# Optimization experiments

Hardware: AMD Instinct MI355X
Metric: run time of the kernel (lower is better)

The kernel has to match this reference:

```python
import jax, jax.numpy as jnp
import numpy as np

NUM_REP = 3

def setup_inputs() -> dict:
    N, E, DIM, R2, L, B, NEG = 20000, 100000, 32, 100, 4, 4, 32
    ks = jax.random.split(jax.random.key(0), 12)
    # all negatives in a row share the same head (required by the model's assert)
    h = jax.random.randint(ks[0], (B, 1), 0, N)
    t = jax.random.randint(ks[1], (B, NEG), 0, N)
    batch = jnp.stack([jnp.broadcast_to(h, (B, NEG)), t], axis=-1)  # [B,NEG,2]
    edge_index = jax.random.randint(ks[2], (2, E), 0, N)
    edge_type = jax.random.randint(ks[3], (E,), 0, R2)
    edge_attr = 0.1 * jax.random.normal(ks[4], (E, DIM), jnp.float32)
    start_query = jax.random.normal(ks[5], (NUM_REP, DIM), jnp.float32)
    W_rel = jax.random.normal(ks[6], (L, DIM, R2 * DIM), jnp.float32) * (DIM ** -0.5)
    b_rel = jnp.zeros((L, R2 * DIM), jnp.float32)
    W_lin = jax.random.normal(ks[7], (L, 2 * DIM, DIM), jnp.float32) * ((2 * DIM) ** -0.5)
    b_lin = jnp.zeros((L, DIM), jnp.float32)
    W_mlp1 = jax.random.normal(ks[8], (DIM, DIM), jnp.float32) * (DIM ** -0.5)
    b_mlp1 = jnp.zeros((DIM,), jnp.float32)
    W_mlp2 = jax.random.normal(ks[9], (DIM, DIM), jnp.float32) * (DIM ** -0.5)
    b_mlp2 = jnp.zeros((DIM,), jnp.float32)
    return {"batch": batch, "edge_index": edge_index, "edge_type": edge_type,
            "edge_attr": edge_attr, "num_nodes": N, "start_query": start_query,
            "W_rel": W_rel, "b_rel": b_rel, "W_lin": W_lin, "b_lin": b_lin,
            "W_mlp1": W_mlp1, "b_mlp1": b_mlp1, "W_mlp2": W_mlp2, "b_mlp2": b_mlp2}

def reference(batch, edge_index, edge_type, edge_attr, num_nodes, start_query,
              W_rel, b_rel, W_lin, b_lin, W_mlp1, b_mlp1, W_mlp2, b_mlp2):
    B, num_neg, _ = batch.shape
    N = int(num_nodes)
    dim = start_query.shape[1]
    L = W_rel.shape[0]
    bs = NUM_REP * B
    batch_full = jnp.tile(batch, (NUM_REP, 1, 1))            # [bs, neg, 2]
    query_idx = jnp.repeat(jnp.arange(NUM_REP), B)           # [bs]
    h_index, t_index = batch_full[..., 0], batch_full[..., 1]
    # negative_sample_to_tail (no-op when heads are constant per row, as built)
    is_t_neg = jnp.all(h_index == h_index[:, :1], axis=-1, keepdims=True)
    h_index, t_index = (jnp.where(is_t_neg, h_index, t_index),
                        jnp.where(is_t_neg, t_index, h_index))
    h0 = h_index[:, 0]
    q = start_query[query_idx]                               # [bs, dim]
    rows = jnp.arange(bs)
    boundary = jnp.zeros((bs, N, dim), q.dtype).at[rows, h0].add(q)
    pb = jnp.zeros((bs, N), q.dtype).at[rows, h0].set(1.0)   # path boundary
    src, dst = edge_index[0], edge_index[1]
    x = boundary
    for l in range(L):
        # dependent per-query relation embeddings: [bs, 2R, dim]
        rel = (q @ W_rel[l] + b_rel[l]).reshape(bs, -1, dim)
        rel_e = rel[:, edge_type] + edge_attr[None]          # [bs, E, dim]
        msg = x[:, src] * rel_e                              # distmult message
        # sum aggregation; boundary acts as the self-loop message
        agg = jnp.zeros((bs, N, dim), x.dtype).at[:, dst].add(msg) + boundary
        x = jax.nn.relu(jnp.concatenate([x, agg], axis=-1) @ W_lin[l] + b_lin[l])
        # reachability propagation of the path boundary (scatter-max)
        pb = jnp.maximum(pb, jnp.zeros((bs, N), pb.dtype).at[:, dst].max(pb[:, src]))
    feat_t = x[rows[:, None], t_index]                       # [bs, neg, dim]
    feat = feat_t.reshape(NUM_REP, B, num_neg, dim).mean(0)  # mean over reps
    features = jax.nn.relu(feat @ W_mlp1 + b_mlp1) @ W_mlp2 + b_mlp2
    pb_t = pb[rows[:, None], t_index][..., None]             # [bs, neg, 1]
    path_boundary = pb_t.reshape(NUM_REP, B, num_neg, 1).max(0)
    return features, path_boundary
```

## Files before the change

### kernel.cpp

```cpp
#include <hip/hip_runtime.h>

#define N_NODES 20000
#define N_EDGES 100000
#define DIM 32
#define R2 100
#define NLAYERS 4
#define BATCH 4
#define NEG 32
#define NREP 3
#define BS (NREP * BATCH)
#define RELDIM (R2 * DIM)

#define NPB 4
#define TPN 96
#define LBLK (NPB * TPN)
#define GRID_LAYER (N_NODES / NPB)

#define XO_A 0
#define XO_B (XO_A + (size_t)N_NODES * BS * DIM)
#define PBO_A (XO_B + (size_t)N_NODES * BS * DIM)
#define PBO_B (PBO_A + (size_t)N_NODES * BS)
#define RELO (PBO_B + (size_t)N_NODES * BS)
#define QO (RELO + (size_t)NLAYERS * R2 * BS * DIM)
#define FLOAT_TOTAL (QO + (size_t)BS * DIM)

#define IO_H0 0
#define IO_TIDX (IO_H0 + BS)
#define IO_COUNTS (IO_TIDX + BS * NEG)
#define IO_OFF (IO_COUNTS + N_NODES)
#define IO_BCUR (IO_OFF + N_NODES + 1)
#define IO_CURSOR (IO_BCUR + 256)
#define IO_ORDER (IO_CURSOR + N_NODES)
#define IO_PAD (IO_ORDER + N_NODES)
#define IO_ES (((IO_PAD + 1) / 2) * 2)
#define INT_TOTAL (IO_ES + 2 * N_EDGES)

__global__ void k_init(const int* __restrict__ batch,
                       const float* __restrict__ start_query,
                       float* __restrict__ q, int* __restrict__ h0,
                       int* __restrict__ t_idx) {
    int r = threadIdx.x;
    if (r >= BS) return;
    int b = r % BATCH, rep = r / BATCH;
    int h00 = batch[(b * NEG + 0) * 2 + 0];
    bool is_t_neg = true;
    for (int j = 0; j < NEG; j++)
        if (batch[(b * NEG + j) * 2 + 0] != h00) { is_t_neg = false; break; }
    int hsel = is_t_neg ? 0 : 1;
    int h0v = batch[(b * NEG + 0) * 2 + hsel];
    h0[r] = h0v;
    for (int j = 0; j < NEG; j++)
        t_idx[r * NEG + j] = batch[(b * NEG + j) * 2 + (1 - hsel)];
    for (int d = 0; d < DIM; d++) q[r * DIM + d] = start_query[rep * DIM + d];
}

__global__ void k_count(const int* __restrict__ dst, int* __restrict__ counts) {
    int e = blockIdx.x * blockDim.x + threadIdx.x;
    if (e < N_EDGES) atomicAdd(&counts[dst[e]], 1);
}

__global__ void k_scan(const int* __restrict__ counts, int* __restrict__ off,
                       int* __restrict__ cursor, int* __restrict__ bcursor) {
    __shared__ int sd[1024];
    __shared__ int hist[256];
    int t = threadIdx.x;
    const int CH = (N_NODES + 1023) / 1024;
    int base = t * CH;
    for (int i = t; i < 256; i += 1024) hist[i] = 0;
    int sum = 0;
    for (int i = 0; i < CH; i++) {
        int idx = base + i;
        if (idx < N_NODES) sum += counts[idx];
    }
    sd[t] = sum;
    __syncthreads();
    for (int o = 1; o < 1024; o <<= 1) {
        int v = (t >= o) ? sd[t - o] : 0;
        __syncthreads();
        sd[t] += v;
        __syncthreads();
    }
    int excl = sd[t] - sum;
    int run = excl;
    for (int i = 0; i < CH; i++) {
        int idx = base + i;
        if (idx < N_NODES) {
            int c = counts[idx];
            off[idx] = run;
            cursor[idx] = run;
            run += c;
            atomicAdd(&hist[c < 255 ? c : 255], 1);
        }
    }
    if (t == 1023) off[N_NODES] = sd[1023];
    __syncthreads();
    if (t == 0) {
        int acc = 0;
        for (int b = 0; b < 256; b++) { bcursor[b] = acc; acc += hist[b]; }
    }
}

__global__ void k_place(const int* __restrict__ src, const int* __restrict__ dst,
                        const int* __restrict__ etype, int* __restrict__ cursor,
                        int2* __restrict__ es) {
    int e = blockIdx.x * blockDim.x + threadIdx.x;
    if (e < N_EDGES) {
        int p = atomicAdd(&cursor[dst[e]], 1);
        es[p] = make_int2(src[e] | (etype[e] << 20), e);
    }
}

__global__ void k_order(const int* __restrict__ counts, int* __restrict__ bcursor,
                        int* __restrict__ node_order) {
    int n = blockIdx.x * blockDim.x + threadIdx.x;
    if (n < N_NODES) {
        int deg = counts[n]; if (deg > 255) deg = 255;
        int pos = atomicAdd(&bcursor[deg], 1);
        node_order[pos] = n;
    }
}

__global__ void k_rel_all(const float* __restrict__ q, const float* __restrict__ W_rel,
                          const float* __restrict__ b_rel, float* __restrict__ rel) {
    int idx = blockIdx.x * blockDim.x + threadIdx.x;
    if (idx >= NLAYERS * R2 * BS * DIM) return;
    int d = idx & 31;
    int r = (idx >> 5) % BS;
    int et = (idx / (BS * DIM)) % R2;
    int l = idx / (R2 * BS * DIM);
    int c = et * DIM + d;
    const float* W = W_rel + (size_t)l * DIM * RELDIM;
    float acc = b_rel[l * RELDIM + c];
    #pragma unroll
    for (int k = 0; k < DIM; k++) acc += q[r * DIM + k] * W[(size_t)k * RELDIM + c];
    rel[idx] = acc;
}

template <bool L0>
__launch_bounds__(LBLK)
__global__ void k_layer(const float* __restrict__ x_old, const float* __restrict__ pb_old,
                        const float* __restrict__ rel_l, const float* __restrict__ edge_attr,
                        const int2* __restrict__ es, const int* __restrict__ off,
                        const int* __restrict__ node_order,
                        const int* __restrict__ h0, const float* __restrict__ q,
                        const float* __restrict__ W_lin_l, const float* __restrict__ b_lin_l,
                        float* __restrict__ x_new, float* __restrict__ pb_new) {
    __shared__ float sW[64 * DIM];
    __shared__ float sB[DIM];
    __shared__ float sIn[NPB * BS * 68];
    __shared__ int sFlag;

    const int gi = threadIdx.x / TPN;
    const int t = threadIdx.x % TPN;
    const int r = t >> 3;
    const int l = t & 7;
    const int n = node_order[blockIdx.x * NPB + gi];

    const int h0r = h0[r];
    const float4 q4 = *(const float4*)(q + r * DIM + l * 4);
    const int s0 = off[n], s1 = off[n + 1];

    if (L0) {
        if (threadIdx.x == 0) sFlag = 0;
        bool spec = (n == h0r);
        for (int k = s0; k < s1; k++) {
            int2 p2 = es[k];
            if ((p2.x & 0xFFFFF) == h0r) spec = true;
        }
        __syncthreads();
        if (spec) sFlag = 1;
        __syncthreads();
        if (!sFlag) {
            float4 b4 = *(const float4*)(b_lin_l + l * 4);
            b4.x = fmaxf(b4.x, 0.f); b4.y = fmaxf(b4.y, 0.f);
            b4.z = fmaxf(b4.z, 0.f); b4.w = fmaxf(b4.w, 0.f);
            *(float4*)(x_new + ((size_t)n * BS + r) * DIM + l * 4) = b4;
            if (l == 0) pb_new[n * BS + r] = 0.f;
            return;
        }
    }

    for (int i = threadIdx.x; i < 64 * DIM; i += LBLK) sW[i] = W_lin_l[i];
    if (threadIdx.x < DIM) sB[threadIdx.x] = b_lin_l[threadIdx.x];

    float4 xr4, ag4 = make_float4(0.f, 0.f, 0.f, 0.f);
    float pbm;
    if (L0) {
        xr4 = (n == h0r) ? q4 : make_float4(0.f, 0.f, 0.f, 0.f);
        pbm = (n == h0r) ? 1.f : 0.f;
    } else {
        xr4 = *(const float4*)(x_old + ((size_t)n * BS + r) * DIM + l * 4);
        pbm = pb_old[n * BS + r];
    }

    for (int k = s0; k < s1; k++) {
        int2 p2 = es[k];
        int s = p2.x & 0xFFFFF;
        int et = ((unsigned)p2.x) >> 20;
        int e = p2.y;
        if (L0) {
            if (s == h0r) {
                float4 rl = *(const float4*)(rel_l + ((size_t)et * BS + r) * DIM + l * 4);
                float4 ea = *(const float4*)(edge_attr + (size_t)e * DIM + l * 4);
                ag4.x += q4.x * (rl.x + ea.x);
                ag4.y += q4.y * (rl.y + ea.y);
                ag4.z += q4.z * (rl.z + ea.z);
                ag4.w += q4.w * (rl.w + ea.w);
                pbm = 1.f;
            }
        } else {
            float4 xs = *(const float4*)(x_old + ((size_t)s * BS + r) * DIM + l * 4);
            float4 rl = *(const float4*)(rel_l + ((size_t)et * BS + r) * DIM + l * 4);
            float4 ea = *(const float4*)(edge_attr + (size_t)e * DIM + l * 4);
            ag4.x += xs.x * (rl.x + ea.x);
            ag4.y += xs.y * (rl.y + ea.y);
            ag4.z += xs.z * (rl.z + ea.z);
            ag4.w += xs.w * (rl.w + ea.w);
            pbm = fmaxf(pbm, pb_old[s * BS + r]);
        }
    }
    if (n == h0r) {
        ag4.x += q4.x; ag4.y += q4.y; ag4.z += q4.z; ag4.w += q4.w;
    }

    float* srow = sIn + (gi * BS + r) * 68;
    *(float4*)(srow + l * 4) = xr4;
    *(float4*)(srow + 32 + l * 4) = ag4;
    __syncthreads();

    float4 acc = *(const float4*)(sB + l * 4);
    #pragma unroll
    for (int k4 = 0; k4 < 16; k4++) {
        float4 v = *(const float4*)(srow + k4 * 4);
        const float* wb = sW + (k4 * 4) * DIM + l * 4;
        float4 w0 = *(const float4*)(wb);
        float4 w1 = *(const float4*)(wb + DIM);
        float4 w2 = *(const float4*)(wb + 2 * DIM);
        float4 w3 = *(const float4*)(wb + 3 * DIM);
        acc.x += v.x * w0.x + v.y * w1.x + v.z * w2.x + v.w * w3.x;
        acc.y += v.x * w0.y + v.y * w1.y + v.z * w2.y + v.w * w3.y;
        acc.z += v.x * w0.z + v.y * w1.z + v.z * w2.z + v.w * w3.z;
        acc.w += v.x * w0.w + v.y * w1.w + v.z * w2.w + v.w * w3.w;
    }
    acc.x = fmaxf(acc.x, 0.f);
    acc.y = fmaxf(acc.y, 0.f);
    acc.z = fmaxf(acc.z, 0.f);
    acc.w = fmaxf(acc.w, 0.f);
    *(float4*)(x_new + ((size_t)n * BS + r) * DIM + l * 4) = acc;
    if (l == 0) pb_new[n * BS + r] = pbm;
}

__launch_bounds__(1024)
__global__ void k_final(const float* __restrict__ x, const float* __restrict__ pb,
                        const int* __restrict__ t_idx,
                        const float* __restrict__ W1, const float* __restrict__ b1,
                        const float* __restrict__ W2, const float* __restrict__ b2,
                        float* __restrict__ out) {
    __shared__ float sW1[DIM * DIM];
    __shared__ float sW2[DIM * DIM];
    __shared__ float sfeat[BATCH * NEG * DIM];
    __shared__ float shid[BATCH * NEG * DIM];
    const int t = threadIdx.x;
    const int NPAIR = BATCH * NEG;

    for (int i = t; i < DIM * DIM; i += 1024) { sW1[i] = W1[i]; sW2[i] = W2[i]; }

    for (int i = t; i < NPAIR * DIM; i += 1024) {
        int pair = i >> 5;
        int d = i & 31;
        int b = pair >> 5;
        int tt = t_idx[pair];
        float s = 0.f;
        #pragma unroll
        for (int rep = 0; rep < NREP; rep++)
            s += x[((size_t)tt * BS + rep * BATCH + b) * DIM + d];
        sfeat[i] = s * (1.f / 3.f);
    }
    __syncthreads();

    for (int i = t; i < NPAIR * DIM; i += 1024) {
        int pair = i >> 5;
        int jj = i & 31;
        float a = b1[jj];
        #pragma unroll
        for (int k = 0; k < DIM; k++)
            a += sfeat[pair * DIM + k] * sW1[k * DIM + jj];
        shid[i] = fmaxf(a, 0.f);
    }
    __syncthreads();

    for (int i = t; i < NPAIR * DIM; i += 1024) {
        int pair = i >> 5;
        int jj = i & 31;
        float a = b2[jj];
        #pragma unroll
        for (int k = 0; k < DIM; k++)
            a += shid[pair * DIM + k] * sW2[k * DIM + jj];
        out[i] = a;
    }

    if (t < NPAIR) {
        int b = t >> 5;
        int tt = t_idx[t];
        float pm = 0.f;
        #pragma unroll
        for (int rep = 0; rep < NREP; rep++)
            pm = fmaxf(pm, pb[(size_t)tt * BS + rep * BATCH + b]);
        out[NPAIR * DIM + t] = pm;
    }
}

extern "C" void kernel_launch(void* const* d_in, const int* in_sizes, int n_in,
                              void* d_out, int out_size, void* d_ws, size_t ws_size,
                              hipStream_t stream) {
    const int* batch = (const int*)d_in[0];
    const int* edge_index = (const int*)d_in[1];
    const int* edge_type = (const int*)d_in[2];
    const float* edge_attr = (const float*)d_in[3];
    const float* start_query = (const float*)d_in[5];
    const float* W_rel = (const float*)d_in[6];
    const float* b_rel = (const float*)d_in[7];
    const float* W_lin = (const float*)d_in[8];
    const float* b_lin = (const float*)d_in[9];
    const float* W_mlp1 = (const float*)d_in[10];
    const float* b_mlp1 = (const float*)d_in[11];
    const float* W_mlp2 = (const float*)d_in[12];
    const float* b_mlp2 = (const float*)d_in[13];

    float* wf = (float*)d_ws;
    int* wi = (int*)(wf + FLOAT_TOTAL);
    size_t need = FLOAT_TOTAL * sizeof(float) + INT_TOTAL * sizeof(int);
    if (ws_size < need) return;

    float* x_a = wf + XO_A;
    float* x_b = wf + XO_B;
    float* pb_a = wf + PBO_A;
    float* pb_b = wf + PBO_B;
    float* rel = wf + RELO;
    float* q = wf + QO;
    int* h0 = wi + IO_H0;
    int* t_idx = wi + IO_TIDX;
    int* counts = wi + IO_COUNTS;
    int* off = wi + IO_OFF;
    int* bcursor = wi + IO_BCUR;
    int* cursor = wi + IO_CURSOR;
    int* node_order = wi + IO_ORDER;
    int2* es = (int2*)(wi + IO_ES);

    const int* src = edge_index;
    const int* dst = edge_index + N_EDGES;

    hipMemsetAsync(counts, 0, (size_t)N_NODES * sizeof(int), stream);

    k_init<<<1, 64, 0, stream>>>(batch, start_query, q, h0, t_idx);

    int eb = (N_EDGES + 255) / 256;
    int nb = (N_NODES + 255) / 256;
    k_count<<<eb, 256, 0, stream>>>(dst, counts);
    k_scan<<<1, 1024, 0, stream>>>(counts, off, cursor, bcursor);
    k_place<<<eb, 256, 0, stream>>>(src, dst, edge_type, cursor, es);
    k_order<<<nb, 256, 0, stream>>>(counts, bcursor, node_order);

    int relb = (NLAYERS * R2 * BS * DIM + 255) / 256;
    k_rel_all<<<relb, 256, 0, stream>>>(q, W_rel, b_rel, rel);

    k_layer<true><<<GRID_LAYER, LBLK, 0, stream>>>(
        x_a, pb_a, rel, edge_attr, es, off, node_order, h0, q,
        W_lin, b_lin, x_a, pb_a);

    float* x_cur = x_a;
    float* x_nxt = x_b;
    float* pb_cur = pb_a;
    float* pb_nxt = pb_b;
    for (int l = 1; l < NLAYERS; l++) {
        k_layer<false><<<GRID_LAYER, LBLK, 0, stream>>>(
            x_cur, pb_cur, rel + (size_t)l * R2 * BS * DIM, edge_attr, es, off,
            node_order, h0, q,
            W_lin + (size_t)l * 64 * DIM, b_lin + (size_t)l * DIM,
            x_nxt, pb_nxt);
        float* tx = x_cur; x_cur = x_nxt; x_nxt = tx;
        float* tp = pb_cur; pb_cur = pb_nxt; pb_nxt = tp;
    }

    k_final<<<1, 1024, 0, stream>>>(x_cur, pb_cur, t_idx, W_mlp1, b_mlp1, W_mlp2, b_mlp2,
                                    (float*)d_out);
}
```

Measured before the change: 393.4 us.

## Merge preprocessing kernels into fewer launches and pad degree bucket counters

Folds the init work into the scan kernel and merges edge placement, node ordering and relation-embedding computation into one block-partitioned prep kernel, cutting the launch count from six to three. Degree bucket cursors are padded to 32-int stride to reduce atomic contention on shared cache lines, and the bucket order is reversed so high-degree nodes come first. The edge loop in the layer kernel also gets unroll 2. The merged kernel mixes heterogeneous block types, which could unbalance the work.

```diff
diff --git a/kernel.cpp b/kernel.cpp
--- a/kernel.cpp
+++ b/kernel.cpp
@@ -16,6 +16,11 @@
 #define LBLK (NPB * TPN)
 #define GRID_LAYER (N_NODES / NPB)
 
+#define EB ((N_EDGES + 255) / 256)
+#define NB ((N_NODES + 255) / 256)
+#define RELB ((NLAYERS * R2 * BS * DIM) / 256)
+#define PREP_GRID (EB + NB + RELB)
+
 #define XO_A 0
 #define XO_B (XO_A + (size_t)N_NODES * BS * DIM)
 #define PBO_A (XO_B + (size_t)N_NODES * BS * DIM)
@@ -29,41 +34,42 @@
 #define IO_COUNTS (IO_TIDX + BS * NEG)
 #define IO_OFF (IO_COUNTS + N_NODES)
 #define IO_BCUR (IO_OFF + N_NODES + 1)
-#define IO_CURSOR (IO_BCUR + 256)
+#define IO_CURSOR (IO_BCUR + 256 * 32)
 #define IO_ORDER (IO_CURSOR + N_NODES)
 #define IO_PAD (IO_ORDER + N_NODES)
 #define IO_ES (((IO_PAD + 1) / 2) * 2)
 #define INT_TOTAL (IO_ES + 2 * N_EDGES)
 
-__global__ void k_init(const int* __restrict__ batch,
+__global__ void k_count(const int* __restrict__ dst, int* __restrict__ counts) {
+    int e = blockIdx.x * blockDim.x + threadIdx.x;
+    if (e < N_EDGES) atomicAdd(&counts[dst[e]], 1);
+}
+
+__global__ void k_scan(const int* __restrict__ counts, int* __restrict__ off,
+                       int* __restrict__ cursor, int* __restrict__ bcursor,
+                       const int* __restrict__ batch,
                        const float* __restrict__ start_query,
                        float* __restrict__ q, int* __restrict__ h0,
                        int* __restrict__ t_idx) {
-    int r = threadIdx.x;
-    if (r >= BS) return;
-    int b = r % BATCH, rep = r / BATCH;
-    int h00 = batch[(b * NEG + 0) * 2 + 0];
-    bool is_t_neg = true;
-    for (int j = 0; j < NEG; j++)
-        if (batch[(b * NEG + j) * 2 + 0] != h00) { is_t_neg = false; break; }
-    int hsel = is_t_neg ? 0 : 1;
-    int h0v = batch[(b * NEG + 0) * 2 + hsel];
-    h0[r] = h0v;
-    for (int j = 0; j < NEG; j++)
-        t_idx[r * NEG + j] = batch[(b * NEG + j) * 2 + (1 - hsel)];
-    for (int d = 0; d < DIM; d++) q[r * DIM + d] = start_query[rep * DIM + d];
-}
-
-__global__ void k_count(const int* __restrict__ dst, int* __restrict__ counts) {
-    int e = blockIdx.x * blockDim.x + threadIdx.x;
-    if (e < N_EDGES) atomicAdd(&counts[dst[e]], 1);
-}
-
-__global__ void k_scan(const int* __restrict__ counts, int* __restrict__ off,
-                       int* __restrict__ cursor, int* __restrict__ bcursor) {
     __shared__ int sd[1024];
     __shared__ int hist[256];
     int t = threadIdx.x;
+
+    if (t < BS) {
+        int r = t;
+        int b = r % BATCH, rep = r / BATCH;
+        int h00 = batch[(b * NEG + 0) * 2 + 0];
+        bool is_t_neg = true;
+        for (int j = 0; j < NEG; j++)
+            if (batch[(b * NEG + j) * 2 + 0] != h00) { is_t_neg = false; break; }
+        int hsel = is_t_neg ? 0 : 1;
+        int h0v = batch[(b * NEG + 0) * 2 + hsel];
+        h0[r] = h0v;
+        for (int j = 0; j < NEG; j++)
+            t_idx[r * NEG + j] = batch[(b * NEG + j) * 2 + (1 - hsel)];
+        for (int d = 0; d < DIM; d++) q[r * DIM + d] = start_query[rep * DIM + d];
+    }
+
     const int CH = (N_NODES + 1023) / 1024;
     int base = t * CH;
     for (int i = t; i < 256; i += 1024) hist[i] = 0;
@@ -96,44 +102,44 @@
     __syncthreads();
     if (t == 0) {
         int acc = 0;
-        for (int b = 0; b < 256; b++) { bcursor[b] = acc; acc += hist[b]; }
-    }
-}
-
-__global__ void k_place(const int* __restrict__ src, const int* __restrict__ dst,
-                        const int* __restrict__ etype, int* __restrict__ cursor,
-                        int2* __restrict__ es) {
-    int e = blockIdx.x * blockDim.x + threadIdx.x;
-    if (e < N_EDGES) {
-        int p = atomicAdd(&cursor[dst[e]], 1);
-        es[p] = make_int2(src[e] | (etype[e] << 20), e);
-    }
-}
-
-__global__ void k_order(const int* __restrict__ counts, int* __restrict__ bcursor,
-                        int* __restrict__ node_order) {
-    int n = blockIdx.x * blockDim.x + threadIdx.x;
-    if (n < N_NODES) {
-        int deg = counts[n]; if (deg > 255) deg = 255;
-        int pos = atomicAdd(&bcursor[deg], 1);
-        node_order[pos] = n;
-    }
-}
-
-__global__ void k_rel_all(const float* __restrict__ q, const float* __restrict__ W_rel,
-                          const float* __restrict__ b_rel, float* __restrict__ rel) {
-    int idx = blockIdx.x * blockDim.x + threadIdx.x;
-    if (idx >= NLAYERS * R2 * BS * DIM) return;
-    int d = idx & 31;
-    int r = (idx >> 5) % BS;
-    int et = (idx / (BS * DIM)) % R2;
-    int l = idx / (R2 * BS * DIM);
-    int c = et * DIM + d;
-    const float* W = W_rel + (size_t)l * DIM * RELDIM;
-    float acc = b_rel[l * RELDIM + c];
-    #pragma unroll
-    for (int k = 0; k < DIM; k++) acc += q[r * DIM + k] * W[(size_t)k * RELDIM + c];
-    rel[idx] = acc;
+        for (int b = 255; b >= 0; b--) { bcursor[b * 32] = acc; acc += hist[b]; }
+    }
+}
+
+__global__ void k_prep(const int* __restrict__ src, const int* __restrict__ dst,
+                       const int* __restrict__ etype, int* __restrict__ cursor,
+                       int2* __restrict__ es,
+                       const int* __restrict__ counts, int* __restrict__ bcursor,
+                       int* __restrict__ node_order,
+                       const float* __restrict__ q, const float* __restrict__ W_rel,
+                       const float* __restrict__ b_rel, float* __restrict__ rel) {
+    int bid = blockIdx.x;
+    if (bid < EB) {
+        int e = bid * 256 + threadIdx.x;
+        if (e < N_EDGES) {
+            int p = atomicAdd(&cursor[dst[e]], 1);
+            es[p] = make_int2(src[e] | (etype[e] << 20), e);
+        }
+    } else if (bid < EB + NB) {
+        int n = (bid - EB) * 256 + threadIdx.x;
+        if (n < N_NODES) {
+            int deg = counts[n]; if (deg > 255) deg = 255;
+            int pos = atomicAdd(&bcursor[deg * 32], 1);
+            node_order[pos] = n;
+        }
+    } else {
+        int idx = (bid - EB - NB) * 256 + threadIdx.x;
+        int d = idx & 31;
+        int r = (idx >> 5) % BS;
+        int et = (idx / (BS * DIM)) % R2;
+        int l = idx / (R2 * BS * DIM);
+        int c = et * DIM + d;
+        const float* W = W_rel + (size_t)l * DIM * RELDIM;
+        float acc = b_rel[l * RELDIM + c];
+        #pragma unroll
+        for (int k = 0; k < DIM; k++) acc += q[r * DIM + k] * W[(size_t)k * RELDIM + c];
+        rel[idx] = acc;
+    }
 }
 
 template <bool L0>
@@ -193,6 +199,7 @@
         pbm = pb_old[n * BS + r];
     }
 
+    #pragma unroll 2
     for (int k = s0; k < s1; k++) {
         int2 p2 = es[k];
         int s = p2.x & 0xFFFFF;
@@ -352,17 +359,12 @@
 
     hipMemsetAsync(counts, 0, (size_t)N_NODES * sizeof(int), stream);
 
-    k_init<<<1, 64, 0, stream>>>(batch, start_query, q, h0, t_idx);
-
-    int eb = (N_EDGES + 255) / 256;
-    int nb = (N_NODES + 255) / 256;
-    k_count<<<eb, 256, 0, stream>>>(dst, counts);
-    k_scan<<<1, 1024, 0, stream>>>(counts, off, cursor, bcursor);
-    k_place<<<eb, 256, 0, stream>>>(src, dst, edge_type, cursor, es);
-    k_order<<<nb, 256, 0, stream>>>(counts, bcursor, node_order);
-
-    int relb = (NLAYERS * R2 * BS * DIM + 255) / 256;
-    k_rel_all<<<relb, 256, 0, stream>>>(q, W_rel, b_rel, rel);
+    k_count<<<EB, 256, 0, stream>>>(dst, counts);
+    k_scan<<<1, 1024, 0, stream>>>(counts, off, cursor, bcursor,
+                                   batch, start_query, q, h0, t_idx);
+    k_prep<<<PREP_GRID, 256, 0, stream>>>(src, dst, edge_type, cursor, es,
+                                          counts, bcursor, node_order,
+                                          q, W_rel, b_rel, rel);
 
     k_layer<true><<<GRID_LAYER, LBLK, 0, stream>>>(
         x_a, pb_a, rel, edge_attr, es, off, node_order, h0, q,
```

New measurement: 345.4 us. -12.2%, faster.
